# Kernel tuning notes

Hardware: AMD Instinct MI355X
Metric: run time of the kernel (lower is better)

The kernel has to match this reference:

```python
import jax, jax.numpy as jnp
import numpy as np

EMBED_DIM = 768

def setup_inputs() -> dict:
    key = jax.random.key(0)
    kx, kq, kk, kv = jax.random.split(key, 4)
    B, T, C = 8, 2048, EMBED_DIM
    scale = 1.0 / np.sqrt(C)
    x = jax.random.normal(kx, (B, T, C), dtype=jnp.float32)
    # nn.Linear weights: out = x @ W.T ; store as [C, C]
    Wq = jax.random.normal(kq, (C, C), dtype=jnp.float32) * scale
    Wk = jax.random.normal(kk, (C, C), dtype=jnp.float32) * scale
    Wv = jax.random.normal(kv, (C, C), dtype=jnp.float32) * scale
    return {"x": x, "Wq": Wq, "Wk": Wk, "Wv": Wv}

def reference(x, Wq, Wk, Wv):
    B, T, C = x.shape
    Q = jnp.einsum('btc,dc->btd', x, Wq)
    K = jnp.einsum('btc,dc->btd', x, Wk)
    V = jnp.einsum('btc,dc->btd', x, Wv)
    scores = jnp.einsum('btd,bsd->bts', Q, K) / jnp.sqrt(jnp.asarray(C, x.dtype))
    causal = jnp.tril(jnp.ones((T, T), dtype=bool))
    scores = jnp.where(causal, scores, -jnp.inf)
    weights = jax.nn.softmax(scores, axis=-1)
    out = jnp.einsum('bts,bsd->btd', weights, V)
    return out
```

## Files before the change

### kernel.cpp

```cpp
#include <hip/hip_runtime.h>
#include <math.h>

#define MM 16384
#define TT 2048
#define BB 8
#define CC 768
#define SOFT_SCALE 0.03608439182435161f

typedef _Float16 f16;
typedef _Float16 half8 __attribute__((ext_vector_type(8)));
typedef _Float16 half4 __attribute__((ext_vector_type(4)));
typedef float f32x4 __attribute__((ext_vector_type(4)));

__device__ __forceinline__ int swz(int r, int cbyte) {
    return r * 128 + (cbyte ^ ((r & 7) << 4));
}

__global__ __launch_bounds__(256) void conv_x(const float* __restrict__ in,
                                              f16* __restrict__ out)
{
    const size_t i = ((size_t)blockIdx.x * 256 + threadIdx.x) * 8;
    float4 a = *(const float4*)(in + i);
    float4 b = *(const float4*)(in + i + 4);
    half8 h;
    h[0]=(f16)a.x; h[1]=(f16)a.y; h[2]=(f16)a.z; h[3]=(f16)a.w;
    h[4]=(f16)b.x; h[5]=(f16)b.y; h[6]=(f16)b.z; h[7]=(f16)b.w;
    *(half8*)(out + i) = h;
}

__global__ __launch_bounds__(256) void conv_w(const float* __restrict__ W0,
                                              const float* __restrict__ W1,
                                              const float* __restrict__ W2,
                                              f16* __restrict__ out)
{
    const int z = blockIdx.y;
    const float* __restrict__ in = (z == 0) ? W0 : (z == 1) ? W1 : W2;
    const size_t i = ((size_t)blockIdx.x * 256 + threadIdx.x) * 8;
    float4 a = *(const float4*)(in + i);
    float4 b = *(const float4*)(in + i + 4);
    half8 h;
    h[0]=(f16)a.x; h[1]=(f16)a.y; h[2]=(f16)a.z; h[3]=(f16)a.w;
    h[4]=(f16)b.x; h[5]=(f16)b.y; h[6]=(f16)b.z; h[7]=(f16)b.w;
    *(half8*)(out + (size_t)z * CC * CC + i) = h;
}

__global__ __launch_bounds__(256) void qkv_gemm_f16(
    const f16* __restrict__ Xh, const f16* __restrict__ Wh,
    f16* __restrict__ Qh, f16* __restrict__ Kh, f16* __restrict__ Vt)
{
    __shared__ char SM[34 * 1024];
    f16* As = (f16*)SM;
    f16* Bs = (f16*)(SM + 16 * 1024);

    const int d = blockIdx.x;
    const int xcd = d & 7, idx = d >> 3;
    const int mt = xcd * 16 + idx / 18;
    const int sub = idx % 18;
    const int z = sub / 6, nt = sub % 6;
    const int m0 = mt * 128, n0 = nt * 128;

    const int tid = threadIdx.x;
    const int lane = tid & 63;
    const int w = tid >> 6;
    const int wr = w >> 1, wc = w & 1;
    const int l15 = lane & 15, lk = lane >> 4;

    f32x4 acc[4][4];
#pragma unroll
    for (int i = 0; i < 4; ++i)
#pragma unroll
        for (int j = 0; j < 4; ++j) acc[i][j] = (f32x4){0.f, 0.f, 0.f, 0.f};

    const int srow = tid >> 1;
    const int scol = (tid & 1) * 32;

    const f16* ga = Xh + (size_t)(m0 + srow) * CC + scol;
    const f16* gb = Wh + (size_t)z * CC * CC + (size_t)(n0 + srow) * CC + scol;

    half8 ra[4], rb[4];
#pragma unroll
    for (int i = 0; i < 4; ++i) {
        ra[i] = *(const half8*)(ga + i * 8);
        rb[i] = *(const half8*)(gb + i * 8);
    }

    for (int k0 = 0; k0 < CC; k0 += 64) {
        __syncthreads();
#pragma unroll
        for (int c = 0; c < 4; ++c) {
            *(half8*)((char*)As + swz(srow, (scol + c * 8) * 2)) = ra[c];
            *(half8*)((char*)Bs + swz(srow, (scol + c * 8) * 2)) = rb[c];
        }
        __syncthreads();
        if (k0 + 64 < CC) {
#pragma unroll
            for (int i = 0; i < 4; ++i) {
                ra[i] = *(const half8*)(ga + (k0 + 64) + i * 8);
                rb[i] = *(const half8*)(gb + (k0 + 64) + i * 8);
            }
        }
#pragma unroll
        for (int kk = 0; kk < 2; ++kk) {
            half8 a[4], b[4];
#pragma unroll
            for (int i = 0; i < 4; ++i)
                a[i] = *(const half8*)((char*)As + swz(wr * 64 + i * 16 + l15, (kk * 32 + lk * 8) * 2));
#pragma unroll
            for (int j = 0; j < 4; ++j)
                b[j] = *(const half8*)((char*)Bs + swz(wc * 64 + j * 16 + l15, (kk * 32 + lk * 8) * 2));
#pragma unroll
            for (int i = 0; i < 4; ++i)
#pragma unroll
                for (int j = 0; j < 4; ++j)
                    acc[i][j] = __builtin_amdgcn_mfma_f32_16x16x32_f16(a[i], b[j], acc[i][j], 0, 0, 0);
        }
    }

    if (z < 2) {
        f16* __restrict__ Y = (z == 0) ? Qh : Kh;
#pragma unroll
        for (int i = 0; i < 4; ++i)
#pragma unroll
            for (int r = 0; r < 4; ++r) {
                int m = m0 + wr * 64 + i * 16 + lk * 4 + r;
#pragma unroll
                for (int j = 0; j < 4; ++j) {
                    int n = n0 + wc * 64 + j * 16 + l15;
                    Y[(size_t)m * CC + n] = (f16)acc[i][j][r];
                }
            }
    } else {
        __syncthreads();
        f16* Bn = (f16*)SM;
#pragma unroll
        for (int i = 0; i < 4; ++i)
#pragma unroll
            for (int j = 0; j < 4; ++j) {
                int n = wc * 64 + j * 16 + l15;
                int m = wr * 64 + i * 16 + lk * 4;
                half4 v;
#pragma unroll
                for (int r = 0; r < 4; ++r) v[r] = (f16)acc[i][j][r];
                *(half4*)&Bn[n * 136 + m] = v;
            }
        __syncthreads();
        const int b  = m0 >> 11;
        const int t0 = m0 & 2047;
        const int nrow = tid >> 1, mc = (tid & 1) * 64;
        f16* dst = Vt + (size_t)b * CC * TT + (size_t)(n0 + nrow) * TT + t0 + mc;
        const f16* src = &Bn[nrow * 136 + mc];
#pragma unroll
        for (int c = 0; c < 8; ++c) *(half8*)(dst + c * 8) = *(const half8*)(src + c * 8);
    }
}

__global__ __launch_bounds__(256) void qk_gemm(
    const f16* __restrict__ Qh, const f16* __restrict__ Kh, f16* __restrict__ S)
{
    const int d = blockIdx.x;
    const int b = d & 7;
    const int tidx = d >> 3;
    int ti = (int)((sqrtf(8.f * tidx + 1.f) - 1.f) * 0.5f);
    while ((ti + 1) * (ti + 2) / 2 <= tidx) ++ti;
    while (ti * (ti + 1) / 2 > tidx) --ti;
    const int tj = tidx - ti * (ti + 1) / 2;

    __shared__ char SM[32 * 1024];
    f16* As = (f16*)SM;
    f16* Bs = (f16*)(SM + 16 * 1024);

    const int tid = threadIdx.x;
    const int m0 = ti * 128, n0 = tj * 128;
    const int lane = tid & 63;
    const int w = tid >> 6;
    const int wr = w >> 1, wc = w & 1;
    const int l15 = lane & 15, lk = lane >> 4;

    f32x4 acc[4][4];
#pragma unroll
    for (int i = 0; i < 4; ++i)
#pragma unroll
        for (int j = 0; j < 4; ++j) acc[i][j] = (f32x4){0.f, 0.f, 0.f, 0.f};

    const int srow = tid >> 1;
    const int scol = (tid & 1) * 32;

    const f16* ga = Qh + (size_t)b * TT * CC + (size_t)(m0 + srow) * CC + scol;
    const f16* gb = Kh + (size_t)b * TT * CC + (size_t)(n0 + srow) * CC + scol;

    half8 ra[4], rb[4];
#pragma unroll
    for (int i = 0; i < 4; ++i) {
        ra[i] = *(const half8*)(ga + i * 8);
        rb[i] = *(const half8*)(gb + i * 8);
    }

    for (int k0 = 0; k0 < CC; k0 += 64) {
        __syncthreads();
#pragma unroll
        for (int c = 0; c < 4; ++c) {
            *(half8*)((char*)As + swz(srow, (scol + c * 8) * 2)) = ra[c];
            *(half8*)((char*)Bs + swz(srow, (scol + c * 8) * 2)) = rb[c];
        }
        __syncthreads();
        if (k0 + 64 < CC) {
#pragma unroll
            for (int i = 0; i < 4; ++i) {
                ra[i] = *(const half8*)(ga + (k0 + 64) + i * 8);
                rb[i] = *(const half8*)(gb + (k0 + 64) + i * 8);
            }
        }
#pragma unroll
        for (int kk = 0; kk < 2; ++kk) {
            half8 a[4], bfr[4];
#pragma unroll
            for (int i = 0; i < 4; ++i)
                a[i] = *(const half8*)((char*)As + swz(wr * 64 + i * 16 + l15, (kk * 32 + lk * 8) * 2));
#pragma unroll
            for (int j = 0; j < 4; ++j)
                bfr[j] = *(const half8*)((char*)Bs + swz(wc * 64 + j * 16 + l15, (kk * 32 + lk * 8) * 2));
#pragma unroll
            for (int i = 0; i < 4; ++i)
#pragma unroll
                for (int j = 0; j < 4; ++j)
                    acc[i][j] = __builtin_amdgcn_mfma_f32_16x16x32_f16(a[i], bfr[j], acc[i][j], 0, 0, 0);
        }
    }

    f16* Sb = S + (size_t)b * TT * TT;
#pragma unroll
    for (int i = 0; i < 4; ++i)
#pragma unroll
        for (int r = 0; r < 4; ++r) {
            int t = m0 + wr * 64 + i * 16 + lk * 4 + r;
#pragma unroll
            for (int j = 0; j < 4; ++j) {
                int s = n0 + wc * 64 + j * 16 + l15;
                Sb[(size_t)t * TT + s] = (f16)(acc[i][j][r] * SOFT_SCALE);
            }
        }
}

__global__ __launch_bounds__(256) void softmax_ker(
    f16* __restrict__ S, float* __restrict__ linv)
{
    const int w = threadIdx.x >> 6, lane = threadIdx.x & 63;
    const int pidx = blockIdx.x * 4 + w;
    const int b = pidx >> 10, q = pidx & 1023;
    f16* Sb = S + (size_t)b * TT * TT;

#pragma unroll
    for (int hh = 0; hh < 2; ++hh) {
        const int t = hh ? (TT - 1 - q) : q;
        f16* row = Sb + (size_t)t * TT;
        const int L = t + 1;

        float m = -1e30f;
        for (int s = lane * 8; s < L; s += 512) {
            half8 v = *(const half8*)(row + s);
#pragma unroll
            for (int j = 0; j < 8; ++j) {
                float f = (float)v[j];
                m = (s + j < L) ? fmaxf(m, f) : m;
            }
        }
#pragma unroll
        for (int o = 32; o >= 1; o >>= 1) m = fmaxf(m, __shfl_xor(m, o));

        float sum = 0.f;
        for (int s = lane * 8; s < L; s += 512) {
            half8 v = *(const half8*)(row + s);
            half8 p;
#pragma unroll
            for (int j = 0; j < 8; ++j) {
                float e = (s + j < L) ? __expf((float)v[j] - m) : 0.f;
                sum += e;
                p[j] = (f16)e;
            }
            *(half8*)(row + s) = p;
        }
#pragma unroll
        for (int o = 32; o >= 1; o >>= 1) sum += __shfl_xor(sum, o);
        if (lane == 0) linv[b * TT + t] = 1.0f / sum;

        const int pe = ((t >> 7) + 1) << 7;
        for (int s = L + lane; s < pe; s += 64) row[s] = (f16)0.f;
    }
}

__global__ __launch_bounds__(256) void pv_gemm(
    const f16* __restrict__ P, const f16* __restrict__ Vt,
    const float* __restrict__ linv, float* __restrict__ O)
{
    const int d = blockIdx.x;
    const int b = d & 7;
    const int r_ = d >> 3;
    const int ti = 15 - r_ / 6;
    const int dj = r_ % 6;

    __shared__ char SM[32 * 1024];
    f16* As = (f16*)SM;
    f16* Bs = (f16*)(SM + 16 * 1024);

    const int tid = threadIdx.x;
    const int m0 = ti * 128, n0 = dj * 128;
    const int lane = tid & 63;
    const int w = tid >> 6;
    const int wr = w >> 1, wc = w & 1;
    const int l15 = lane & 15, lk = lane >> 4;

    f32x4 acc[4][4];
#pragma unroll
    for (int i = 0; i < 4; ++i)
#pragma unroll
        for (int j = 0; j < 4; ++j) acc[i][j] = (f32x4){0.f, 0.f, 0.f, 0.f};

    const int srow = tid >> 1;
    const int scol = (tid & 1) * 32;
    const int KE = (ti + 1) * 128;

    const f16* ga = P  + (size_t)b * TT * TT + (size_t)(m0 + srow) * TT + scol;
    const f16* gb = Vt + (size_t)b * CC * TT + (size_t)(n0 + srow) * TT + scol;

    half8 ra[4], rb[4];
#pragma unroll
    for (int i = 0; i < 4; ++i) {
        ra[i] = *(const half8*)(ga + i * 8);
        rb[i] = *(const half8*)(gb + i * 8);
    }

    for (int k0 = 0; k0 < KE; k0 += 64) {
        __syncthreads();
#pragma unroll
        for (int c = 0; c < 4; ++c) {
            *(half8*)((char*)As + swz(srow, (scol + c * 8) * 2)) = ra[c];
            *(half8*)((char*)Bs + swz(srow, (scol + c * 8) * 2)) = rb[c];
        }
        __syncthreads();
        if (k0 + 64 < KE) {
#pragma unroll
            for (int i = 0; i < 4; ++i) {
                ra[i] = *(const half8*)(ga + (k0 + 64) + i * 8);
                rb[i] = *(const half8*)(gb + (k0 + 64) + i * 8);
            }
        }
#pragma unroll
        for (int kk = 0; kk < 2; ++kk) {
            half8 a[4], bfr[4];
#pragma unroll
            for (int i = 0; i < 4; ++i)
                a[i] = *(const half8*)((char*)As + swz(wr * 64 + i * 16 + l15, (kk * 32 + lk * 8) * 2));
#pragma unroll
            for (int j = 0; j < 4; ++j)
                bfr[j] = *(const half8*)((char*)Bs + swz(wc * 64 + j * 16 + l15, (kk * 32 + lk * 8) * 2));
#pragma unroll
            for (int i = 0; i < 4; ++i)
#pragma unroll
                for (int j = 0; j < 4; ++j)
                    acc[i][j] = __builtin_amdgcn_mfma_f32_16x16x32_f16(a[i], bfr[j], acc[i][j], 0, 0, 0);
        }
    }

    float* Ob = O + (size_t)b * TT * CC;
#pragma unroll
    for (int i = 0; i < 4; ++i)
#pragma unroll
        for (int r = 0; r < 4; ++r) {
            int t = m0 + wr * 64 + i * 16 + lk * 4 + r;
            float sc = linv[b * TT + t];
#pragma unroll
            for (int j = 0; j < 4; ++j) {
                int dd = n0 + wc * 64 + j * 16 + l15;
                Ob[(size_t)t * CC + dd] = acc[i][j][r] * sc;
            }
        }
}

extern "C" void kernel_launch(void* const* d_in, const int* in_sizes, int n_in,
                              void* d_out, int out_size, void* d_ws, size_t ws_size,
                              hipStream_t stream) {
    (void)in_sizes; (void)n_in; (void)out_size; (void)ws_size;
    const float* x  = (const float*)d_in[0];
    const float* Wq = (const float*)d_in[1];
    const float* Wk = (const float*)d_in[2];
    const float* Wv = (const float*)d_in[3];

    f16* Qh = (f16*)d_ws;
    f16* Kh = Qh + (size_t)MM * CC;
    f16* Vt = Kh + (size_t)MM * CC;
    f16* S  = Vt + (size_t)MM * CC;
    float* linv = (float*)(S + (size_t)BB * TT * TT);
    f16* Xh = S;
    f16* Wh = S + (size_t)MM * CC;
    float* out = (float*)d_out;

    conv_x      <<<6144, 256, 0, stream>>>(x, Xh);
    conv_w      <<<dim3(288, 3), 256, 0, stream>>>(Wq, Wk, Wv, Wh);
    qkv_gemm_f16<<<2304, 256, 0, stream>>>(Xh, Wh, Qh, Kh, Vt);
    qk_gemm     <<<1088, 256, 0, stream>>>(Qh, Kh, S);
    softmax_ker <<<2048, 256, 0, stream>>>(S, linv);
    pv_gemm     <<<768,  256, 0, stream>>>(S, Vt, linv, out);
}
```

Baseline: 286.0 us.

## Use direct global-to-LDS loads in all three GEMM kernels

Replaces the register-staged global load plus LDS store pipeline with __builtin_amdgcn_global_load_lds 16-byte loads that write straight into shared memory. The XOR swizzle moves into the global column address so the LDS layout matches the existing swz reads. This cuts VGPR use and the separate ds_write instructions. It also drops the register prefetch of the next tile, so global latency is no longer overlapped with MFMA work inside a block.

Measured after the change: 278.7 us. -2.5%, faster.

```diff
diff --git a/kernel.cpp b/kernel.cpp
--- a/kernel.cpp
+++ b/kernel.cpp
@@ -14,6 +14,13 @@
 
 __device__ __forceinline__ int swz(int r, int cbyte) {
     return r * 128 + (cbyte ^ ((r & 7) << 4));
+}
+
+__device__ __forceinline__ void gload16(const void* g, void* l) {
+    __builtin_amdgcn_global_load_lds(
+        (const __attribute__((address_space(1))) void*)g,
+        (__attribute__((address_space(3))) void*)l,
+        16, 0, 0);
 }
 
 __global__ __launch_bounds__(256) void conv_x(const float* __restrict__ in,
@@ -71,34 +78,20 @@
 #pragma unroll
         for (int j = 0; j < 4; ++j) acc[i][j] = (f32x4){0.f, 0.f, 0.f, 0.f};
 
-    const int srow = tid >> 1;
-    const int scol = (tid & 1) * 32;
-
-    const f16* ga = Xh + (size_t)(m0 + srow) * CC + scol;
-    const f16* gb = Wh + (size_t)z * CC * CC + (size_t)(n0 + srow) * CC + scol;
-
-    half8 ra[4], rb[4];
-#pragma unroll
-    for (int i = 0; i < 4; ++i) {
-        ra[i] = *(const half8*)(ga + i * 8);
-        rb[i] = *(const half8*)(gb + i * 8);
-    }
+    const int srow8 = lane >> 3;
+    const int xcol  = ((lane & 7) ^ srow8) * 8;
+
+    const f16* ga = Xh + (size_t)(m0 + w * 32 + srow8) * CC + xcol;
+    const f16* gb = Wh + (size_t)z * CC * CC + (size_t)(n0 + w * 32 + srow8) * CC + xcol;
 
     for (int k0 = 0; k0 < CC; k0 += 64) {
         __syncthreads();
 #pragma unroll
         for (int c = 0; c < 4; ++c) {
-            *(half8*)((char*)As + swz(srow, (scol + c * 8) * 2)) = ra[c];
-            *(half8*)((char*)Bs + swz(srow, (scol + c * 8) * 2)) = rb[c];
-        }
-        __syncthreads();
-        if (k0 + 64 < CC) {
-#pragma unroll
-            for (int i = 0; i < 4; ++i) {
-                ra[i] = *(const half8*)(ga + (k0 + 64) + i * 8);
-                rb[i] = *(const half8*)(gb + (k0 + 64) + i * 8);
-            }
-        }
+            gload16(ga + (size_t)c * 8 * CC + k0, (char*)SM + (w * 4 + c) * 1024);
+            gload16(gb + (size_t)c * 8 * CC + k0, (char*)SM + 16 * 1024 + (w * 4 + c) * 1024);
+        }
+        __syncthreads();
 #pragma unroll
         for (int kk = 0; kk < 2; ++kk) {
             half8 a[4], b[4];
@@ -182,34 +175,20 @@
 #pragma unroll
         for (int j = 0; j < 4; ++j) acc[i][j] = (f32x4){0.f, 0.f, 0.f, 0.f};
 
-    const int srow = tid >> 1;
-    const int scol = (tid & 1) * 32;
-
-    const f16* ga = Qh + (size_t)b * TT * CC + (size_t)(m0 + srow) * CC + scol;
-    const f16* gb = Kh + (size_t)b * TT * CC + (size_t)(n0 + srow) * CC + scol;
-
-    half8 ra[4], rb[4];
-#pragma unroll
-    for (int i = 0; i < 4; ++i) {
-        ra[i] = *(const half8*)(ga + i * 8);
-        rb[i] = *(const half8*)(gb + i * 8);
-    }
+    const int srow8 = lane >> 3;
+    const int xcol  = ((lane & 7) ^ srow8) * 8;
+
+    const f16* ga = Qh + (size_t)b * TT * CC + (size_t)(m0 + w * 32 + srow8) * CC + xcol;
+    const f16* gb = Kh + (size_t)b * TT * CC + (size_t)(n0 + w * 32 + srow8) * CC + xcol;
 
     for (int k0 = 0; k0 < CC; k0 += 64) {
         __syncthreads();
 #pragma unroll
         for (int c = 0; c < 4; ++c) {
-            *(half8*)((char*)As + swz(srow, (scol + c * 8) * 2)) = ra[c];
-            *(half8*)((char*)Bs + swz(srow, (scol + c * 8) * 2)) = rb[c];
-        }
-        __syncthreads();
-        if (k0 + 64 < CC) {
-#pragma unroll
-            for (int i = 0; i < 4; ++i) {
-                ra[i] = *(const half8*)(ga + (k0 + 64) + i * 8);
-                rb[i] = *(const half8*)(gb + (k0 + 64) + i * 8);
-            }
-        }
+            gload16(ga + (size_t)c * 8 * CC + k0, (char*)SM + (w * 4 + c) * 1024);
+            gload16(gb + (size_t)c * 8 * CC + k0, (char*)SM + 16 * 1024 + (w * 4 + c) * 1024);
+        }
+        __syncthreads();
 #pragma unroll
         for (int kk = 0; kk < 2; ++kk) {
             half8 a[4], bfr[4];
@@ -315,35 +294,21 @@
 #pragma unroll
         for (int j = 0; j < 4; ++j) acc[i][j] = (f32x4){0.f, 0.f, 0.f, 0.f};
 
-    const int srow = tid >> 1;
-    const int scol = (tid & 1) * 32;
+    const int srow8 = lane >> 3;
+    const int xcol  = ((lane & 7) ^ srow8) * 8;
     const int KE = (ti + 1) * 128;
 
-    const f16* ga = P  + (size_t)b * TT * TT + (size_t)(m0 + srow) * TT + scol;
-    const f16* gb = Vt + (size_t)b * CC * TT + (size_t)(n0 + srow) * TT + scol;
-
-    half8 ra[4], rb[4];
-#pragma unroll
-    for (int i = 0; i < 4; ++i) {
-        ra[i] = *(const half8*)(ga + i * 8);
-        rb[i] = *(const half8*)(gb + i * 8);
-    }
+    const f16* ga = P  + (size_t)b * TT * TT + (size_t)(m0 + w * 32 + srow8) * TT + xcol;
+    const f16* gb = Vt + (size_t)b * CC * TT + (size_t)(n0 + w * 32 + srow8) * TT + xcol;
 
     for (int k0 = 0; k0 < KE; k0 += 64) {
         __syncthreads();
 #pragma unroll
         for (int c = 0; c < 4; ++c) {
-            *(half8*)((char*)As + swz(srow, (scol + c * 8) * 2)) = ra[c];
-            *(half8*)((char*)Bs + swz(srow, (scol + c * 8) * 2)) = rb[c];
-        }
-        __syncthreads();
-        if (k0 + 64 < KE) {
-#pragma unroll
-            for (int i = 0; i < 4; ++i) {
-                ra[i] = *(const half8*)(ga + (k0 + 64) + i * 8);
-                rb[i] = *(const half8*)(gb + (k0 + 64) + i * 8);
-            }
-        }
+            gload16(ga + (size_t)c * 8 * TT + k0, (char*)SM + (w * 4 + c) * 1024);
+            gload16(gb + (size_t)c * 8 * TT + k0, (char*)SM + 16 * 1024 + (w * 4 + c) * 1024);
+        }
+        __syncthreads();
 #pragma unroll
         for (int kk = 0; kk < 2; ++kk) {
             half8 a[4], bfr[4];
```
